# Optimization experiments

Measured on AMD Instinct MI355X. Metric: run time of the kernel, lower is better.

Reference implementation:

```python
import jax, jax.numpy as jnp
import numpy as np

EMBED_DIM = 1280
NUM_HEADS = 20
HEAD_DIM = EMBED_DIM // NUM_HEADS  # 64
TGT_LEN = 2048
BSZ = 2
SCALING = HEAD_DIM ** -0.5


def setup_inputs() -> dict:
    key = jax.random.key(0)
    ks = jax.random.split(key, 6)
    s = EMBED_DIM ** -0.5
    query = jax.random.normal(ks[0], (TGT_LEN, BSZ, EMBED_DIM), dtype=jnp.float32)
    Wq = jax.random.normal(ks[1], (EMBED_DIM, EMBED_DIM), dtype=jnp.float32) * s
    Wk = jax.random.normal(ks[2], (EMBED_DIM, EMBED_DIM), dtype=jnp.float32) * s
    Wv = jax.random.normal(ks[3], (EMBED_DIM, EMBED_DIM), dtype=jnp.float32) * s
    Wo = jax.random.normal(ks[4], (EMBED_DIM, EMBED_DIM), dtype=jnp.float32) * s
    bq = jnp.zeros((EMBED_DIM,), jnp.float32)
    bk = jnp.zeros((EMBED_DIM,), jnp.float32)
    bv = jnp.zeros((EMBED_DIM,), jnp.float32)
    bo = jnp.zeros((EMBED_DIM,), jnp.float32)
    # key_padding_mask: (bsz, src_len), True = padded; pad last 256 keys of batch 1
    kpm = np.zeros((BSZ, TGT_LEN), dtype=bool)
    kpm[1, -256:] = True
    key_padding_mask = jnp.asarray(kpm)
    return {"query": query, "key_padding_mask": key_padding_mask,
            "Wq": Wq, "bq": bq, "Wk": Wk, "bk": bk,
            "Wv": Wv, "bv": bv, "Wo": Wo, "bo": bo}


def _mha(query, key_padding_mask, Wq, bq, Wk, bk, Wv, bv, Wo, bo):
    T, B, E = query.shape
    H, D = NUM_HEADS, HEAD_DIM
    q = (query @ Wq + bq) * SCALING            # [T, B, E]
    k = query @ Wk + bk
    v = query @ Wv + bv
    # reshape to [B*H, T, D] as in the TF code
    q = q.reshape(T, B * H, D).transpose(1, 0, 2)
    k = k.reshape(T, B * H, D).transpose(1, 0, 2)
    v = v.reshape(T, B * H, D).transpose(1, 0, 2)
    attn_weights = jnp.einsum('bqd,bkd->bqk', q, k)   # [B*H, T, T]
    # key padding mask: (B, src_len), 1s excluded -> -inf
    aw = attn_weights.reshape(B, H, T, T)
    aw = jnp.where(key_padding_mask[:, None, None, :], -jnp.inf, aw)
    attn_weights_float = jax.nn.softmax(aw.astype(jnp.float32).reshape(B * H, T, T), axis=-1)
    attn_probs = attn_weights_float.astype(v.dtype)  # dropout rate 0.0 -> identity
    attn = jnp.einsum('bqk,bkd->bqd', attn_probs, v)  # [B*H, T, D]
    attn = attn.transpose(1, 0, 2).reshape(T, B, E)
    attn = attn @ Wo + bo
    # need_weights=True (default), need_head_weights=False -> mean over heads
    avg_weights = attn_weights_float.reshape(B, H, T, T).transpose(1, 0, 2, 3).mean(axis=0)
    return attn, avg_weights


def reference(query, key_padding_mask, Wq, bq, Wk, bk, Wv, bv, Wo, bo):
    return _mha(query, key_padding_mask, Wq, bq, Wk, bk, Wv, bv, Wo, bo)
```

## Files before the change

kernel.cpp:

```cpp
#include <hip/hip_runtime.h>

#define T_LEN 2048
#define BSZ   2
#define EMB   1280
#define NH    20
#define HD    64
#define NBH   (BSZ*NH)
#define NR    (T_LEN*BSZ)
#define QSCALE (0.125f * 1.4426950408889634f)

#define KPAD 68

typedef short bf16x8 __attribute__((ext_vector_type(8)));
typedef short bf16x4 __attribute__((ext_vector_type(4)));
typedef float f32x4  __attribute__((ext_vector_type(4)));

__device__ inline short f2bf(float f) {
    union { float f; unsigned u; } v; v.f = f;
    unsigned u = v.u + 0x7FFF + ((v.u >> 16) & 1);
    return (short)(u >> 16);
}

__device__ inline unsigned cvt_pk_bf16(float lo, float hi) {
    unsigned r;
    asm("v_cvt_pk_bf16_f32 %0, %1, %2" : "=v"(r) : "v"(lo), "v"(hi));
    return r;
}

__device__ inline void glds16(const short* g, short* l) {
    __builtin_amdgcn_global_load_lds(
        (const __attribute__((address_space(1))) void*)g,
        (__attribute__((address_space(3))) void*)l,
        16, 0, 0);
}

__global__ __launch_bounds__(256) void k_cvt_x(
    const float* __restrict__ X, short* __restrict__ Xb)
{
    size_t i0 = ((size_t)blockIdx.x*256 + threadIdx.x) * 8;
    float4 a = *(const float4*)(X + i0);
    float4 b = *(const float4*)(X + i0 + 4);
    bf16x8 r = { f2bf(a.x), f2bf(a.y), f2bf(a.z), f2bf(a.w),
                 f2bf(b.x), f2bf(b.y), f2bf(b.z), f2bf(b.w) };
    *(bf16x8*)(Xb + i0) = r;
}

__global__ __launch_bounds__(256) void k_cvt_wt(
    const float* __restrict__ Wq, const float* __restrict__ Wk,
    const float* __restrict__ Wv, const float* __restrict__ Wo,
    short* __restrict__ Wqt, short* __restrict__ Wkt,
    short* __restrict__ Wvt, short* __restrict__ Wot)
{
    const int z = blockIdx.z;
    const float* __restrict__ W = (z==0)?Wq:(z==1)?Wk:(z==2)?Wv:Wo;
    short* __restrict__ Wt      = (z==0)?Wqt:(z==1)?Wkt:(z==2)?Wvt:Wot;

    const int k0 = blockIdx.y * 32;
    const int n0 = blockIdx.x * 32;
    const int t  = threadIdx.x;

    __shared__ float Ls[32][33];
    {
        int row = t >> 3, col = (t & 7) * 4;
        *(float4*)&Ls[row][col] = *(const float4*)(W + (size_t)(k0+row)*EMB + n0 + col);
    }
    __syncthreads();
    {
        int n = t >> 3, k4 = (t & 7) * 4;
        bf16x4 r = { f2bf(Ls[k4+0][n]), f2bf(Ls[k4+1][n]),
                     f2bf(Ls[k4+2][n]), f2bf(Ls[k4+3][n]) };
        *(bf16x4*)(Wt + (size_t)(n0+n)*EMB + k0 + k4) = r;
    }
}

__global__ __launch_bounds__(256) void k_gemm_qkv(
    const short* __restrict__ Xb,
    const short* __restrict__ Wqt, const short* __restrict__ Wkt, const short* __restrict__ Wvt,
    const float* __restrict__ bq, const float* __restrict__ bk, const float* __restrict__ bv,
    short* __restrict__ Qb, short* __restrict__ Kb, short* __restrict__ Vt)
{
    const int which = blockIdx.z;
    const short* __restrict__ Wt   = (which==0) ? Wqt : (which==1) ? Wkt : Wvt;
    const float* __restrict__ bias = (which==0) ? bq  : (which==1) ? bk  : bv;
    const float scale = (which==0) ? QSCALE : 1.0f;

    const int bm = blockIdx.y * 128;
    const int bn = blockIdx.x * 128;
    const int t    = threadIdx.x;
    const int wave = t >> 6, lane = t & 63;
    const int l16  = lane & 15, quad = lane >> 4;
    const int wm   = (wave >> 1) * 64, wn = (wave & 1) * 64;

    __shared__ short As[128][64];
    __shared__ short Bs[128][64];

    const int srow   = lane >> 3;
    const int scolsw = (((lane & 7) ^ srow) & 7) * 8;
    const int rsw    = (l16 & 7) << 3;

    f32x4 acc[4][4] = {};

    for (int kt = 0; kt < EMB; kt += 64) {
        __syncthreads();
        const short* Ag = Xb + (size_t)bm*EMB + kt;
        const short* Bg = Wt + (size_t)bn*EMB + kt;
        #pragma unroll
        for (int c = 0; c < 4; ++c) {
            int seg = wave*4 + c;
            int grow = seg*8 + srow;
            glds16(Ag + (size_t)grow*EMB + scolsw, &As[seg*8][0]);
            glds16(Bg + (size_t)grow*EMB + scolsw, &Bs[seg*8][0]);
        }
        __syncthreads();
        #pragma unroll
        for (int ks = 0; ks < 64; ks += 32) {
            bf16x8 af[4], bfr[4];
            #pragma unroll
            for (int mi=0;mi<4;++mi) af[mi]  = *(const bf16x8*)&As[wm + mi*16 + l16][(ks + quad*8) ^ rsw];
            #pragma unroll
            for (int ni=0;ni<4;++ni) bfr[ni] = *(const bf16x8*)&Bs[wn + ni*16 + l16][(ks + quad*8) ^ rsw];
            #pragma unroll
            for (int mi=0;mi<4;++mi)
                #pragma unroll
                for (int ni=0;ni<4;++ni)
                    acc[mi][ni] = __builtin_amdgcn_mfma_f32_16x16x32_bf16(af[mi], bfr[ni], acc[mi][ni], 0,0,0);
        }
    }

    #pragma unroll
    for (int ni=0;ni<4;++ni) {
        int c = bn + wn + ni*16 + l16;
        float bval = bias[c];
        int h = c >> 6, d = c & 63;
        #pragma unroll
        for (int mi=0;mi<4;++mi) {
            #pragma unroll
            for (int j=0;j<4;++j) {
                int r = bm + wm + mi*16 + quad*4 + j;
                int tt = r >> 1, bb = r & 1;
                float val = (acc[mi][ni][j] + bval) * scale;
                if (which == 2)
                    Vt[((size_t)(bb*NH+h)*HD + d)*T_LEN + tt] = f2bf(val);
                else {
                    short* dst = (which==0) ? Qb : Kb;
                    dst[((size_t)(bb*NH+h)*T_LEN + tt)*HD + d] = f2bf(val);
                }
            }
        }
    }
}

__global__ __launch_bounds__(512) void k_pv(
    const short* __restrict__ Qb, const short* __restrict__ Kb, const short* __restrict__ Vt,
    const int* __restrict__ kpm,
    float* __restrict__ Linv,
    short* __restrict__ AttnMidb)
{
    const int qt = blockIdx.x;
    const int bh = blockIdx.y;
    const int b  = bh / NH, h = bh % NH;
    const int t    = threadIdx.x;
    const int w    = t >> 6;
    const int lane = t & 63;
    const int l16  = lane & 15;
    const int quad = lane >> 4;
    const int q0   = qt*128 + w*16;

    __shared__ short Ks[2][64][KPAD];
    __shared__ short Vts[2][64][KPAD];
    __shared__ float MfL[2][64];
    __shared__ float Lsh[128];

    bf16x8 qf[2];
    #pragma unroll
    for (int ch=0;ch<2;++ch)
        qf[ch] = *(const bf16x8*)(Qb + ((size_t)bh*T_LEN + q0 + l16)*HD + ch*32 + quad*8);

    const int row0 = t >> 3, col8 = (t & 7) * 8;
    const short* Kgb = Kb + (size_t)bh*T_LEN*HD;
    const short* Vgb = Vt + (size_t)bh*HD*T_LEN;

    *(bf16x8*)&Ks[0][row0][col8]  = *(const bf16x8*)(Kgb + (size_t)row0*HD + col8);
    *(bf16x8*)&Vts[0][row0][col8] = *(const bf16x8*)(Vgb + (size_t)row0*T_LEN + col8);
    if (t < 64) MfL[0][t] = kpm[b*T_LEN + t] ? 0.f : 1.f;
    __syncthreads();

    f32x4 o[4] = {};
    float l = 0.f;
    int cur = 0;

    for (int kt = 0; kt < T_LEN; kt += 64) {
        const int ktn = kt + 64;
        const bool has_next = ktn < T_LEN;
        const int nxt = cur ^ 1;

        bf16x8 kr0, vr0;
        float mfn = 0.f;
        if (has_next) {
            kr0 = *(const bf16x8*)(Kgb + (size_t)(ktn + row0)*HD + col8);
            vr0 = *(const bf16x8*)(Vgb + (size_t)row0*T_LEN + ktn + col8);
            if (t < 64) mfn = kpm[b*T_LEN + ktn + t] ? 0.f : 1.f;
        }

        f32x4 s[4] = {};
        #pragma unroll
        for (int ch = 0; ch < 2; ++ch) {
            bf16x8 ka[4];
            #pragma unroll
            for (int mb=0;mb<4;++mb) ka[mb] = *(const bf16x8*)&Ks[cur][mb*16 + l16][ch*32 + quad*8];
            #pragma unroll
            for (int mb=0;mb<4;++mb)
                s[mb] = __builtin_amdgcn_mfma_f32_16x16x32_bf16(ka[mb], qf[ch], s[mb], 0,0,0);
        }

        unsigned pu[2][4];
        #pragma unroll
        for (int c = 0; c < 2; ++c) {
            #pragma unroll
            for (int mb2 = 0; mb2 < 2; ++mb2) {
                const int mb = c*2 + mb2;
                float4 mf = *(const float4*)&MfL[cur][mb*16 + quad*4];
                float p0 = __builtin_amdgcn_exp2f(s[mb][0]) * mf.x;
                float p1 = __builtin_amdgcn_exp2f(s[mb][1]) * mf.y;
                float p2 = __builtin_amdgcn_exp2f(s[mb][2]) * mf.z;
                float p3 = __builtin_amdgcn_exp2f(s[mb][3]) * mf.w;
                l += (p0 + p1) + (p2 + p3);
                pu[c][mb2*2+0] = cvt_pk_bf16(p0, p1);
                pu[c][mb2*2+1] = cvt_pk_bf16(p2, p3);
            }
        }

        if (has_next) {
            *(bf16x8*)&Ks[nxt][row0][col8]  = kr0;
            *(bf16x8*)&Vts[nxt][row0][col8] = vr0;
            if (t < 64) MfL[nxt][t] = mfn;
        }

        #pragma unroll
        for (int c = 0; c < 2; ++c) {
            bf16x8 vv[4];
            #pragma unroll
            for (int nb=0;nb<4;++nb) {
                bf16x4 va = *(const bf16x4*)&Vts[cur][nb*16 + l16][c*32 + quad*4];
                bf16x4 vb = *(const bf16x4*)&Vts[cur][nb*16 + l16][c*32 + 16 + quad*4];
                vv[nb] = (bf16x8){va[0],va[1],va[2],va[3], vb[0],vb[1],vb[2],vb[3]};
            }
            union { unsigned u[4]; bf16x8 v; } pa;
            pa.u[0]=pu[c][0]; pa.u[1]=pu[c][1];
            pa.u[2]=pu[c][2]; pa.u[3]=pu[c][3];
            #pragma unroll
            for (int nb=0;nb<4;++nb)
                o[nb] = __builtin_amdgcn_mfma_f32_16x16x32_bf16(pa.v, vv[nb], o[nb], 0,0,0);
        }

        __syncthreads();
        cur = nxt;
    }

    l += __shfl_xor(l, 16);
    l += __shfl_xor(l, 32);
    float linv = 1.0f / l;
    if (quad == 0) {
        Linv[(size_t)bh*T_LEN + q0 + l16] = linv;
        Lsh[w*16 + l16] = linv;
    }
    {
        float4 li = *(const float4*)&Lsh[w*16 + quad*4];
        float lr[4] = {li.x, li.y, li.z, li.w};
        #pragma unroll
        for (int r=0;r<4;++r) {
            int q = q0 + quad*4 + r;
            size_t base = ((size_t)q*BSZ + b)*EMB + h*HD;
            #pragma unroll
            for (int nb=0;nb<4;++nb)
                AttnMidb[base + nb*16 + l16] = f2bf(o[nb][r] * lr[r]);
        }
    }
}

__global__ __launch_bounds__(256) void k_meanw(
    const short* __restrict__ Qb, const short* __restrict__ Kb,
    const int* __restrict__ kpm,
    const float* __restrict__ Linv,
    float* __restrict__ avg)
{
    const int kt = blockIdx.x;
    const int qt = blockIdx.y;
    const int b  = blockIdx.z;
    const int t    = threadIdx.x;
    const int wave = t >> 6, lane = t & 63;
    const int l16  = lane & 15, quad = lane >> 4;

    __shared__ short Qs[64][KPAD];
    __shared__ short Ks[64][KPAD];
    __shared__ float Lish[64];
    __shared__ int   msk[64];

    if (t < 64) msk[t] = kpm[b*T_LEN + kt*64 + t];

    f32x4 acc[4] = {};
    const int qrow_in = wave*16 + quad*4;

    for (int h = 0; h < NH; ++h) {
        const int bh = b*NH + h;
        __syncthreads();
        {
            const short* Qg = Qb + ((size_t)bh*T_LEN + qt*64)*HD;
            const short* Kg = Kb + ((size_t)bh*T_LEN + kt*64)*HD;
            #pragma unroll
            for (int c = 0; c < 2; ++c) {
                int idx = c*256 + t;
                int row = idx >> 3, col8 = (idx & 7) * 8;
                *(bf16x8*)&Qs[row][col8] = *(const bf16x8*)(Qg + (size_t)row*HD + col8);
                *(bf16x8*)&Ks[row][col8] = *(const bf16x8*)(Kg + (size_t)row*HD + col8);
            }
        }
        if (t < 64) Lish[t] = Linv[(size_t)bh*T_LEN + qt*64 + t];
        __syncthreads();

        bf16x8 aq0 = *(const bf16x8*)&Qs[wave*16 + l16][quad*8];
        bf16x8 aq1 = *(const bf16x8*)&Qs[wave*16 + l16][32 + quad*8];

        float lv[4];
        #pragma unroll
        for (int r = 0; r < 4; ++r)
            lv[r] = Lish[qrow_in + r] * (1.0f/NH);

        #pragma unroll
        for (int nb = 0; nb < 4; ++nb) {
            bf16x8 bk0 = *(const bf16x8*)&Ks[nb*16 + l16][quad*8];
            bf16x8 bk1 = *(const bf16x8*)&Ks[nb*16 + l16][32 + quad*8];
            f32x4 s = {};
            s = __builtin_amdgcn_mfma_f32_16x16x32_bf16(aq0, bk0, s, 0,0,0);
            s = __builtin_amdgcn_mfma_f32_16x16x32_bf16(aq1, bk1, s, 0,0,0);
            const bool mk = msk[nb*16 + l16] != 0;
            #pragma unroll
            for (int r = 0; r < 4; ++r)
                acc[nb][r] += mk ? 0.f : __builtin_amdgcn_exp2f(s[r]) * lv[r];
        }
    }

    #pragma unroll
    for (int r = 0; r < 4; ++r) {
        int q = qt*64 + qrow_in + r;
        size_t base = ((size_t)b*T_LEN + q) * T_LEN + (size_t)kt*64;
        #pragma unroll
        for (int nb = 0; nb < 4; ++nb)
            avg[base + nb*16 + l16] = acc[nb][r];
    }
}

__global__ __launch_bounds__(256) void k_gemm_out(
    const short* __restrict__ Ab, const short* __restrict__ Wot,
    const float* __restrict__ bo, float* __restrict__ out)
{
    const int bm = blockIdx.y * 128;
    const int bn = blockIdx.x * 128;
    const int t    = threadIdx.x;
    const int wave = t >> 6, lane = t & 63;
    const int l16  = lane & 15, quad = lane >> 4;
    const int wm   = (wave >> 1) * 64, wn = (wave & 1) * 64;

    __shared__ short As[128][64];
    __shared__ short Bs[128][64];

    const int srow   = lane >> 3;
    const int scolsw = (((lane & 7) ^ srow) & 7) * 8;
    const int rsw    = (l16 & 7) << 3;

    f32x4 acc[4][4] = {};

    for (int kt = 0; kt < EMB; kt += 64) {
        __syncthreads();
        const short* Ag = Ab  + (size_t)bm*EMB + kt;
        const short* Bg = Wot + (size_t)bn*EMB + kt;
        #pragma unroll
        for (int c = 0; c < 4; ++c) {
            int seg = wave*4 + c;
            int grow = seg*8 + srow;
            glds16(Ag + (size_t)grow*EMB + scolsw, &As[seg*8][0]);
            glds16(Bg + (size_t)grow*EMB + scolsw, &Bs[seg*8][0]);
        }
        __syncthreads();
        #pragma unroll
        for (int ks = 0; ks < 64; ks += 32) {
            bf16x8 af[4], bfr[4];
            #pragma unroll
            for (int mi=0;mi<4;++mi) af[mi]  = *(const bf16x8*)&As[wm + mi*16 + l16][(ks + quad*8) ^ rsw];
            #pragma unroll
            for (int ni=0;ni<4;++ni) bfr[ni] = *(const bf16x8*)&Bs[wn + ni*16 + l16][(ks + quad*8) ^ rsw];
            #pragma unroll
            for (int mi=0;mi<4;++mi)
                #pragma unroll
                for (int ni=0;ni<4;++ni)
                    acc[mi][ni] = __builtin_amdgcn_mfma_f32_16x16x32_bf16(af[mi], bfr[ni], acc[mi][ni], 0,0,0);
        }
    }

    #pragma unroll
    for (int ni=0;ni<4;++ni) {
        int c = bn + wn + ni*16 + l16;
        float bval = bo[c];
        #pragma unroll
        for (int mi=0;mi<4;++mi) {
            #pragma unroll
            for (int j=0;j<4;++j) {
                int r = bm + wm + mi*16 + quad*4 + j;
                out[(size_t)r*EMB + c] = acc[mi][ni][j] + bval;
            }
        }
    }
}

extern "C" void kernel_launch(void* const* d_in, const int* in_sizes, int n_in,
                              void* d_out, int out_size, void* d_ws, size_t ws_size,
                              hipStream_t stream) {
    const float* X   = (const float*)d_in[0];
    const int*   kpm = (const int*)  d_in[1];
    const float* Wq  = (const float*)d_in[2];
    const float* bq  = (const float*)d_in[3];
    const float* Wk  = (const float*)d_in[4];
    const float* bk  = (const float*)d_in[5];
    const float* Wv  = (const float*)d_in[6];
    const float* bv  = (const float*)d_in[7];
    const float* Wo  = (const float*)d_in[8];
    const float* bo  = (const float*)d_in[9];

    float* out = (float*)d_out;
    float* ws  = (float*)d_ws;

    const size_t QKV = (size_t)NBH * T_LEN * HD;
    float* Linv = ws;
    short* Xb   = (short*)(Linv + (size_t)NBH * T_LEN);
    short* Wqt  = Xb  + (size_t)NR * EMB;
    short* Wkt  = Wqt + (size_t)EMB * EMB;
    short* Wvt  = Wkt + (size_t)EMB * EMB;
    short* Wot  = Wvt + (size_t)EMB * EMB;
    short* Qb   = Wot + (size_t)EMB * EMB;
    short* Kb   = Qb  + QKV;
    short* Vt   = Kb  + QKV;
    short* Amid = Vt  + QKV;

    float* attn_out = out;
    float* avg      = out + (size_t)T_LEN * BSZ * EMB;

    k_cvt_x   <<<dim3((NR*EMB)/(256*8)), 256, 0, stream>>>(X, Xb);
    k_cvt_wt  <<<dim3(EMB/32, EMB/32, 4), 256, 0, stream>>>(Wq, Wk, Wv, Wo, Wqt, Wkt, Wvt, Wot);
    k_gemm_qkv<<<dim3(EMB/128, NR/128, 3), 256, 0, stream>>>(Xb, Wqt, Wkt, Wvt, bq, bk, bv, Qb, Kb, Vt);
    k_pv      <<<dim3(T_LEN/128, NBH),   512, 0, stream>>>(Qb, Kb, Vt, kpm, Linv, Amid);
    k_meanw   <<<dim3(T_LEN/64, T_LEN/64, BSZ), 256, 0, stream>>>(Qb, Kb, kpm, Linv, avg);
    k_gemm_out<<<dim3(EMB/128, NR/128),  256, 0, stream>>>(Amid, Wot, bo, attn_out);
}
```

Baseline: 345.8 us.

## Double-buffer per-head Q/K tiles in mean-weights kernel and remap block order

The mean-weights kernel now prefetches the next head's Q and K tiles and the Linv values into registers while computing the current head from a double-buffered LDS tile. This halves the barriers per head and hides global load latency behind the MFMA and exp work. Both the PV and mean-weights kernels also remap the linear block index with a stride-8 swizzle, presumably to spread neighbouring blocks across XCDs for L2 locality. The cost is more LDS and register pressure, and the remap hardcodes the grid sizes.

```diff
diff --git a/kernel.cpp b/kernel.cpp
--- a/kernel.cpp
+++ b/kernel.cpp
@@ -156,8 +156,10 @@
     float* __restrict__ Linv,
     short* __restrict__ AttnMidb)
 {
-    const int qt = blockIdx.x;
-    const int bh = blockIdx.y;
+    int lin = blockIdx.y*gridDim.x + blockIdx.x;
+    lin = (lin & 7) * 80 + (lin >> 3);
+    const int qt = lin & 15;
+    const int bh = lin >> 4;
     const int b  = bh / NH, h = bh % NH;
     const int t    = threadIdx.x;
     const int w    = t >> 6;
@@ -284,52 +286,68 @@
     const float* __restrict__ Linv,
     float* __restrict__ avg)
 {
-    const int kt = blockIdx.x;
-    const int qt = blockIdx.y;
-    const int b  = blockIdx.z;
+    int lin = (blockIdx.z*gridDim.y + blockIdx.y)*gridDim.x + blockIdx.x;
+    lin = (lin & 7) * 256 + (lin >> 3);
+    const int kt = lin & 31;
+    const int qt = (lin >> 5) & 31;
+    const int b  = lin >> 10;
+
     const int t    = threadIdx.x;
     const int wave = t >> 6, lane = t & 63;
     const int l16  = lane & 15, quad = lane >> 4;
 
-    __shared__ short Qs[64][KPAD];
-    __shared__ short Ks[64][KPAD];
-    __shared__ float Lish[64];
+    __shared__ short Qs[2][64][KPAD];
+    __shared__ short Ks[2][64][KPAD];
+    __shared__ float Lish[2][64];
     __shared__ int   msk[64];
 
+    const int srow = t >> 2;
+    const int scol = (t & 3) * 16;
+
+    const short* Qg0 = Qb + ((size_t)(b*NH)*T_LEN + qt*64)*HD;
+    const short* Kg0 = Kb + ((size_t)(b*NH)*T_LEN + kt*64)*HD;
+    const size_t hstride = (size_t)T_LEN*HD;
+
     if (t < 64) msk[t] = kpm[b*T_LEN + kt*64 + t];
+
+    *(bf16x8*)&Qs[0][srow][scol]   = *(const bf16x8*)(Qg0 + (size_t)srow*HD + scol);
+    *(bf16x8*)&Qs[0][srow][scol+8] = *(const bf16x8*)(Qg0 + (size_t)srow*HD + scol + 8);
+    *(bf16x8*)&Ks[0][srow][scol]   = *(const bf16x8*)(Kg0 + (size_t)srow*HD + scol);
+    *(bf16x8*)&Ks[0][srow][scol+8] = *(const bf16x8*)(Kg0 + (size_t)srow*HD + scol + 8);
+    if (t < 64) Lish[0][t] = Linv[(size_t)(b*NH)*T_LEN + qt*64 + t];
+    __syncthreads();
 
     f32x4 acc[4] = {};
     const int qrow_in = wave*16 + quad*4;
+    int cur = 0;
 
     for (int h = 0; h < NH; ++h) {
-        const int bh = b*NH + h;
-        __syncthreads();
-        {
-            const short* Qg = Qb + ((size_t)bh*T_LEN + qt*64)*HD;
-            const short* Kg = Kb + ((size_t)bh*T_LEN + kt*64)*HD;
-            #pragma unroll
-            for (int c = 0; c < 2; ++c) {
-                int idx = c*256 + t;
-                int row = idx >> 3, col8 = (idx & 7) * 8;
-                *(bf16x8*)&Qs[row][col8] = *(const bf16x8*)(Qg + (size_t)row*HD + col8);
-                *(bf16x8*)&Ks[row][col8] = *(const bf16x8*)(Kg + (size_t)row*HD + col8);
-            }
-        }
-        if (t < 64) Lish[t] = Linv[(size_t)bh*T_LEN + qt*64 + t];
-        __syncthreads();
-
-        bf16x8 aq0 = *(const bf16x8*)&Qs[wave*16 + l16][quad*8];
-        bf16x8 aq1 = *(const bf16x8*)&Qs[wave*16 + l16][32 + quad*8];
+        const int nxt = cur ^ 1;
+
+        bf16x8 qr0, qr1, kr0, kr1;
+        float lnx = 0.f;
+        if (h+1 < NH) {
+            const short* Qg = Qg0 + (size_t)(h+1)*hstride;
+            const short* Kg = Kg0 + (size_t)(h+1)*hstride;
+            qr0 = *(const bf16x8*)(Qg + (size_t)srow*HD + scol);
+            qr1 = *(const bf16x8*)(Qg + (size_t)srow*HD + scol + 8);
+            kr0 = *(const bf16x8*)(Kg + (size_t)srow*HD + scol);
+            kr1 = *(const bf16x8*)(Kg + (size_t)srow*HD + scol + 8);
+            if (t < 64) lnx = Linv[(size_t)(b*NH + h+1)*T_LEN + qt*64 + t];
+        }
+
+        bf16x8 aq0 = *(const bf16x8*)&Qs[cur][wave*16 + l16][quad*8];
+        bf16x8 aq1 = *(const bf16x8*)&Qs[cur][wave*16 + l16][32 + quad*8];
 
         float lv[4];
         #pragma unroll
         for (int r = 0; r < 4; ++r)
-            lv[r] = Lish[qrow_in + r] * (1.0f/NH);
+            lv[r] = Lish[cur][qrow_in + r] * (1.0f/NH);
 
         #pragma unroll
         for (int nb = 0; nb < 4; ++nb) {
-            bf16x8 bk0 = *(const bf16x8*)&Ks[nb*16 + l16][quad*8];
-            bf16x8 bk1 = *(const bf16x8*)&Ks[nb*16 + l16][32 + quad*8];
+            bf16x8 bk0 = *(const bf16x8*)&Ks[cur][nb*16 + l16][quad*8];
+            bf16x8 bk1 = *(const bf16x8*)&Ks[cur][nb*16 + l16][32 + quad*8];
             f32x4 s = {};
             s = __builtin_amdgcn_mfma_f32_16x16x32_bf16(aq0, bk0, s, 0,0,0);
             s = __builtin_amdgcn_mfma_f32_16x16x32_bf16(aq1, bk1, s, 0,0,0);
@@ -338,6 +356,16 @@
             for (int r = 0; r < 4; ++r)
                 acc[nb][r] += mk ? 0.f : __builtin_amdgcn_exp2f(s[r]) * lv[r];
         }
+
+        if (h+1 < NH) {
+            *(bf16x8*)&Qs[nxt][srow][scol]   = qr0;
+            *(bf16x8*)&Qs[nxt][srow][scol+8] = qr1;
+            *(bf16x8*)&Ks[nxt][srow][scol]   = kr0;
+            *(bf16x8*)&Ks[nxt][srow][scol+8] = kr1;
+            if (t < 64) Lish[nxt][t] = lnx;
+        }
+        __syncthreads();
+        cur = nxt;
     }
 
     #pragma unroll
```

Measured after the change: 341.4 us, median of 2. No clear change (-1.3%).
